# Performance work log

Hardware: AMD Instinct MI355X
Metric: run time of the kernel (lower is better)

## Reference

```python
import jax, jax.numpy as jnp
import numpy as np

B, S, IN_DIM = 8, 1024, 512
EMBED_DIM, NUM_HEADS = 512, 8
HEAD_DIM = EMBED_DIM // NUM_HEADS
LN_EPS = 1e-5


def setup_inputs() -> dict:
    key = jax.random.key(0)
    k1, k2, k3 = jax.random.split(key, 3)
    x = jax.random.normal(k1, (B, S, IN_DIM), dtype=jnp.float32)
    # xavier_uniform for qkv_proj.weight [3*embed, in] and o_proj.weight [embed, embed]
    lim_qkv = float(np.sqrt(6.0 / (3 * EMBED_DIM + IN_DIM)))
    w_qkv = jax.random.uniform(k2, (3 * EMBED_DIM, IN_DIM), dtype=jnp.float32,
                               minval=-lim_qkv, maxval=lim_qkv)
    lim_o = float(np.sqrt(6.0 / (EMBED_DIM + EMBED_DIM)))
    w_o = jax.random.uniform(k3, (EMBED_DIM, EMBED_DIM), dtype=jnp.float32,
                             minval=-lim_o, maxval=lim_o)
    return {"x": x, "w_qkv": w_qkv, "w_o": w_o}


def reference(x, w_qkv, w_o):
    b, s, _ = x.shape
    # fused QKV projection: [b, s, 3*embed]
    qkv = jnp.einsum('bsi,ei->bse', x, w_qkv)
    # [b, h, s, 3*head_dim]
    qkv = qkv.reshape(b, s, NUM_HEADS, 3 * HEAD_DIM).transpose(0, 2, 1, 3)
    q, k, v = jnp.split(qkv, 3, axis=-1)
    scale = 1.0 / np.sqrt(HEAD_DIM)
    logits = jnp.einsum('bhqd,bhkd->bhqk', q, k) * scale  # [b, h, s, s]
    attn = jax.nn.softmax(logits, axis=-1)
    vals = jnp.einsum('bhqk,bhkd->bhqd', attn, v)
    vals = vals.transpose(0, 2, 1, 3).reshape(b, s, EMBED_DIM)
    o = jnp.einsum('bse,fe->bsf', vals, w_o)
    # LayerNorm over [seq, embed] jointly (fresh nn.LayerNorm([N, D]): weight=1, bias=0)
    mu = jnp.mean(o, axis=(-2, -1), keepdims=True)
    var = jnp.var(o, axis=(-2, -1), keepdims=True)
    o = (o - mu) / jnp.sqrt(var + LN_EPS)
    return o
```

## Files before the change

kernel.cpp:

```cpp
#include <hip/hip_runtime.h>
#include <hip/hip_bf16.h>
#include <math.h>

#define BB 8
#define SS 1024
#define INDIM 512
#define ED 512
#define NH 8
#define HD 64

typedef __attribute__((ext_vector_type(8))) short short8;
typedef __attribute__((ext_vector_type(4))) float f32x4;
typedef __attribute__((ext_vector_type(16))) float f32x16;
typedef unsigned short u16;

typedef __attribute__((address_space(1))) const void gv_t;
typedef __attribute__((address_space(3))) void lv_t;

static __device__ __forceinline__ u16 f2bf(float f) {
  union { float f; unsigned u; } v; v.f = f;
  unsigned r = v.u + 0x7fffu + ((v.u >> 16) & 1u);
  return (u16)(r >> 16);
}

static __device__ __forceinline__ unsigned cvt_pk_bf16(float a, float b) {
  unsigned r;
  asm("v_cvt_pk_bf16_f32 %0, %1, %2" : "=v"(r) : "v"(a), "v"(b));
  return r;
}
static __device__ __forceinline__ float fast_exp2(float x) {
  float r; asm("v_exp_f32 %0, %1" : "=v"(r) : "v"(x)); return r;
}

__global__ void cvt_all(const float* __restrict__ x, const float* __restrict__ wq,
                        const float* __restrict__ wo, u16* __restrict__ xb,
                        u16* __restrict__ wqb, u16* __restrict__ wob) {
  const int n1 = 1048576;
  const int n2 = n1 + 196608;
  const int n3 = n2 + 65536;
  int i = blockIdx.x * blockDim.x + threadIdx.x;
  int stride = gridDim.x * blockDim.x;
  for (; i < n3; i += stride) {
    const float4* src; ushort4* dst; int j;
    if (i < n1)      { src = (const float4*)x;  dst = (ushort4*)xb;  j = i; }
    else if (i < n2) { src = (const float4*)wq; dst = (ushort4*)wqb; j = i - n1; }
    else             { src = (const float4*)wo; dst = (ushort4*)wob; j = i - n2; }
    float4 v = src[j];
    ushort4 o;
    o.x = f2bf(v.x); o.y = f2bf(v.y); o.z = f2bf(v.z); o.w = f2bf(v.w);
    dst[j] = o;
  }
}

template<int EPI>
__global__ __launch_bounds__(256, 2)
void gemm_nt(const u16* __restrict__ A, const u16* __restrict__ Bm, int K,
             float* __restrict__ outF,
             u16* __restrict__ qws, u16* __restrict__ kws, u16* __restrict__ vtws,
             float2* __restrict__ partials)
{
  __shared__ u16 As[128][64];
  __shared__ u16 Bs[128][64];
  const int tid = threadIdx.x;
  const int lane = tid & 63;
  const int wv = tid >> 6;
  const int wr = wv >> 1, wc = wv & 1;
  const int bm = blockIdx.x, bn = blockIdx.y;
  const int l15 = lane & 15, lg = lane >> 4;
  const int srow8 = lane >> 3;
  const int sc8 = lane & 7;

  f32x4 acc[4][4];
  #pragma unroll
  for (int i = 0; i < 4; i++)
    #pragma unroll
    for (int j = 0; j < 4; j++) acc[i][j] = (f32x4){0.f, 0.f, 0.f, 0.f};

  for (int kk = 0; kk < K; kk += 64) {
    #pragma unroll
    for (int i = 0; i < 4; i++) {
      int r0 = (i * 4 + wv) * 8;
      int r = r0 + srow8;
      int cs = sc8 ^ (r & 7);
      const u16* ga = A + (size_t)(bm * 128 + r) * K + kk + cs * 8;
      __builtin_amdgcn_global_load_lds((gv_t*)ga, (lv_t*)&As[r0][0], 16, 0, 0);
      const u16* gb = Bm + (size_t)(bn * 128 + r) * K + kk + cs * 8;
      __builtin_amdgcn_global_load_lds((gv_t*)gb, (lv_t*)&Bs[r0][0], 16, 0, 0);
    }
    __syncthreads();
    #pragma unroll
    for (int kc = 0; kc < 2; kc++) {
      short8 af[4], bf[4];
      #pragma unroll
      for (int mi = 0; mi < 4; mi++) {
        int ra = wr * 64 + mi * 16 + l15;
        af[mi] = *(const short8*)&As[ra][((kc * 4 + lg) ^ (ra & 7)) * 8];
      }
      #pragma unroll
      for (int ni = 0; ni < 4; ni++) {
        int rb = wc * 64 + ni * 16 + l15;
        bf[ni] = *(const short8*)&Bs[rb][((kc * 4 + lg) ^ (rb & 7)) * 8];
      }
      #pragma unroll
      for (int mi = 0; mi < 4; mi++)
        #pragma unroll
        for (int ni = 0; ni < 4; ni++)
          acc[mi][ni] = __builtin_amdgcn_mfma_f32_16x16x32_bf16(af[mi], bf[ni], acc[mi][ni], 0, 0, 0);
    }
    __syncthreads();
  }

  if (EPI == 0) {
    #pragma unroll
    for (int mi = 0; mi < 4; mi++) {
      int rowg = bm * 128 + wr * 64 + mi * 16 + lg * 4;
      #pragma unroll
      for (int ni = 0; ni < 4; ni++) {
        int colg = bn * 128 + wc * 64 + ni * 16 + l15;
        #pragma unroll
        for (int r = 0; r < 4; r++) {
          int rg = rowg + r;
          float v = acc[mi][ni][r];
          int b = rg >> 10, s = rg & 1023;
          int h = colg / 192, c = colg - h * 192;
          int bh = b * 8 + h;
          if (c < 64)
            qws[((size_t)(bh * 1024 + s)) * 64 + c] = f2bf(v * 0.18033688f);
          else if (c < 128)
            kws[((size_t)(bh * 1024 + s)) * 64 + (c - 64)] = f2bf(v);
          else
            vtws[((size_t)(bh * 64 + (c - 128))) * 1024 + s] = f2bf(v);
        }
      }
    }
  } else {
    float s1 = 0.f, s2 = 0.f;
    #pragma unroll
    for (int mi = 0; mi < 4; mi++) {
      int rowg = bm * 128 + wr * 64 + mi * 16 + lg * 4;
      #pragma unroll
      for (int ni = 0; ni < 4; ni++) {
        int colg = bn * 128 + wc * 64 + ni * 16 + l15;
        #pragma unroll
        for (int r = 0; r < 4; r++) {
          float v = acc[mi][ni][r];
          s1 += v; s2 += v * v;
          outF[(size_t)(rowg + r) * 512 + colg] = v;
        }
      }
    }
    #pragma unroll
    for (int off = 1; off < 64; off <<= 1) {
      s1 += __shfl_xor(s1, off);
      s2 += __shfl_xor(s2, off);
    }
    __shared__ float r1[4], r2[4];
    if (lane == 0) { r1[wv] = s1; r2[wv] = s2; }
    __syncthreads();
    if (tid == 0) {
      float t1 = r1[0] + r1[1] + r1[2] + r1[3];
      float t2 = r2[0] + r2[1] + r2[2] + r2[3];
      partials[bm * 4 + bn] = make_float2(t1, t2);
    }
  }
}

__global__ __launch_bounds__(512, 4)
void attn_kernel(const u16* __restrict__ qws, const u16* __restrict__ kws,
                 const u16* __restrict__ vtws, u16* __restrict__ vals)
{
  __shared__ __align__(16) u16 Ksm[2][64][72];
  __shared__ __align__(16) u16 Vsm[2][64][72];
  const int tid = threadIdx.x;
  const int lane = tid & 63;
  const int wq = tid >> 6;
  const int l31 = lane & 31;
  const int hi = lane >> 5;
  const int logical = (blockIdx.x & 7) * 32 + (blockIdx.x >> 3);
  const int bh = logical >> 2;
  const int q0 = (logical & 3) * 256;

  short8 qf[4];
  {
    const u16* qp = qws + ((size_t)bh * 1024 + q0 + wq * 32 + l31) * 64 + 8 * hi;
    #pragma unroll
    for (int j = 0; j < 4; j++) qf[j] = *(const short8*)(qp + 16 * j);
  }

  const int srow = tid >> 3;
  const int sc8 = (tid & 7) * 8;
  uint4 kreg, vreg;
  kreg = *(const uint4*)(kws + ((size_t)bh * 1024 + srow) * 64 + sc8);
  vreg = *(const uint4*)(vtws + ((size_t)(bh * 64 + srow)) * 1024 + sc8);
  *(uint4*)&Ksm[0][srow][sc8] = kreg;
  *(uint4*)&Vsm[0][srow][sc8] = vreg;
  __syncthreads();

  f32x16 o[2];
  #pragma unroll
  for (int r = 0; r < 16; r++) { o[0][r] = 0.f; o[1][r] = 0.f; }
  float m = -1e30f, l = 0.f;

  for (int t = 0; t < 16; t++) {
    const int cur = t & 1;
    if (t < 15) {
      int kv = (t + 1) * 64;
      kreg = *(const uint4*)(kws + ((size_t)bh * 1024 + kv + srow) * 64 + sc8);
      vreg = *(const uint4*)(vtws + ((size_t)(bh * 64 + srow)) * 1024 + kv + sc8);
    }

    f32x16 stv[2];
    __builtin_amdgcn_s_setprio(1);
    #pragma unroll
    for (int s2 = 0; s2 < 2; s2++) {
      f32x16 c;
      #pragma unroll
      for (int r = 0; r < 16; r++) c[r] = 0.f;
      #pragma unroll
      for (int j = 0; j < 4; j++) {
        short8 kf = *(const short8*)&Ksm[cur][s2 * 32 + l31][16 * j + 8 * hi];
        c = __builtin_amdgcn_mfma_f32_32x32x16_bf16(kf, qf[j], c, 0, 0, 0);
      }
      stv[s2] = c;
    }
    __builtin_amdgcn_s_setprio(0);

    float mx[16];
    #pragma unroll
    for (int r = 0; r < 16; r++) mx[r] = fmaxf(stv[0][r], stv[1][r]);
    #pragma unroll
    for (int w = 8; w >= 1; w >>= 1)
      #pragma unroll
      for (int r = 0; r < w; r++) mx[r] = fmaxf(mx[r], mx[r + w]);
    float pm = fmaxf(mx[0], __shfl_xor(mx[0], 32));

    if (!__all(pm - m <= 10.0f)) {
      float mn = fmaxf(m, pm);
      float al = fast_exp2(m - mn);
      m = mn; l *= al;
      #pragma unroll
      for (int reg = 0; reg < 16; reg++) {
        int qrow = (reg & 3) + 8 * (reg >> 2) + 4 * hi;
        float alo = __shfl(al, qrow);
        o[0][reg] *= alo; o[1][reg] *= alo;
      }
    }

    unsigned pk[16];
    float ps[16];
    #pragma unroll
    for (int s2 = 0; s2 < 2; s2++)
      #pragma unroll
      for (int j = 0; j < 8; j++) {
        float p0 = fast_exp2(stv[s2][2 * j] - m);
        float p1 = fast_exp2(stv[s2][2 * j + 1] - m);
        ps[s2 * 8 + j] = p0 + p1;
        pk[s2 * 8 + j] = cvt_pk_bf16(p0, p1);
      }
    #pragma unroll
    for (int w = 8; w >= 1; w >>= 1)
      #pragma unroll
      for (int r = 0; r < w; r++) ps[r] += ps[r + w];
    l += ps[0] + __shfl_xor(ps[0], 32);

    short8 pa[4];
    #pragma unroll
    for (int cc = 0; cc < 4; cc++) {
      int base = (cc >> 1) * 8 + (cc & 1) * 4;
      unsigned a0 = pk[base + 0], a2 = pk[base + 2];
      unsigned a1 = pk[base + 1], a3 = pk[base + 3];
      asm volatile("v_permlane32_swap_b32 %0, %1" : "+v"(a0), "+v"(a2));
      asm volatile("v_permlane32_swap_b32 %0, %1" : "+v"(a1), "+v"(a3));
      union { unsigned u[4]; short8 s8; } uu;
      uu.u[0] = a0; uu.u[1] = a1; uu.u[2] = a2; uu.u[3] = a3;
      pa[cc] = uu.s8;
    }

    __builtin_amdgcn_s_setprio(1);
    #pragma unroll
    for (int dh = 0; dh < 2; dh++)
      #pragma unroll
      for (int cc = 0; cc < 4; cc++) {
        short8 vf = *(const short8*)&Vsm[cur][dh * 32 + l31][16 * cc + 8 * hi];
        o[dh] = __builtin_amdgcn_mfma_f32_32x32x16_bf16(pa[cc], vf, o[dh], 0, 0, 0);
      }
    __builtin_amdgcn_s_setprio(0);

    if (t < 15) {
      *(uint4*)&Ksm[cur ^ 1][srow][sc8] = kreg;
      *(uint4*)&Vsm[cur ^ 1][srow][sc8] = vreg;
    }
    __syncthreads();
  }

  const int b = bh >> 3, h = bh & 7;
  #pragma unroll
  for (int reg = 0; reg < 16; reg++) {
    int qrow = (reg & 3) + 8 * (reg >> 2) + 4 * hi;
    float linv = 1.0f / __shfl(l, qrow);
    size_t grow = (size_t)(b * 1024 + q0 + wq * 32 + qrow) * 512 + h * 64;
    vals[grow + l31]      = f2bf(o[0][reg] * linv);
    vals[grow + 32 + l31] = f2bf(o[1][reg] * linv);
  }
}

__global__ void ln_norm2(float* __restrict__ o, const float2* __restrict__ partials) {
  const int blk = blockIdx.x;
  const int b = blk >> 8;
  const int lane = threadIdx.x & 63;
  float s1 = 0.f, s2 = 0.f;
  if (lane < 32) {
    float2 p = partials[b * 32 + lane];
    s1 = p.x; s2 = p.y;
  }
  #pragma unroll
  for (int off = 1; off < 64; off <<= 1) {
    s1 += __shfl_xor(s1, off);
    s2 += __shfl_xor(s2, off);
  }
  float mu = s1 / 524288.f;
  float rs = rsqrtf(s2 / 524288.f - mu * mu + 1e-5f);
  const int base = blk * 512;
  #pragma unroll
  for (int k = 0; k < 2; k++) {
    int i = base + threadIdx.x + k * 256;
    float4 v = ((const float4*)o)[i];
    v.x = (v.x - mu) * rs; v.y = (v.y - mu) * rs;
    v.z = (v.z - mu) * rs; v.w = (v.w - mu) * rs;
    ((float4*)o)[i] = v;
  }
}

extern "C" void kernel_launch(void* const* d_in, const int* in_sizes, int n_in,
                              void* d_out, int out_size, void* d_ws, size_t ws_size,
                              hipStream_t stream) {
  const float* x = (const float*)d_in[0];
  const float* wqkv = (const float*)d_in[1];
  const float* wo = (const float*)d_in[2];
  float* out = (float*)d_out;
  char* ws = (char*)d_ws;

  u16* xb        = (u16*)(ws + 0);
  u16* wqb       = (u16*)(ws + 8388608);
  u16* wob       = (u16*)(ws + 9961472);
  u16* qws       = (u16*)(ws + 10485760);
  u16* kws       = (u16*)(ws + 18874368);
  u16* vtws      = (u16*)(ws + 27262976);
  u16* vals      = (u16*)(ws + 35651584);
  float2* parts  = (float2*)(ws + 44040192);

  cvt_all<<<1280, 256, 0, stream>>>(x, wqkv, wo, xb, wqb, wob);

  dim3 g1(64, 12);
  gemm_nt<0><<<g1, 256, 0, stream>>>(xb, wqb, 512, nullptr, qws, kws, vtws, nullptr);

  attn_kernel<<<256, 512, 0, stream>>>(qws, kws, vtws, vals);

  dim3 g2(64, 4);
  gemm_nt<1><<<g2, 256, 0, stream>>>(vals, wob, 512, out, nullptr, nullptr, nullptr, parts);

  ln_norm2<<<2048, 256, 0, stream>>>(out, parts);
}
```

Before: 82.75 us.

## Double attention KV tile to 128 keys and interleave softmax with PV MFMAs

The attention kernel now processes 128 keys per iteration instead of 64, which halves the number of loop iterations and __syncthreads barriers and enlarges the double-buffered K/V shared-memory tiles. The exp/pack/PV work is split into per-32-key chunks so that probability conversion and PV MFMAs interleave, which keeps register pressure bounded. In exchange the kernel uses more LDS and registers, and launch bounds drop from 4 to 2 blocks per CU, so occupancy is lower.

Result: slower. 88.88 us (+7.4%).

```diff
diff --git a/kernel.cpp b/kernel.cpp
--- a/kernel.cpp
+++ b/kernel.cpp
@@ -165,12 +165,12 @@
   }
 }
 
-__global__ __launch_bounds__(512, 4)
+__global__ __launch_bounds__(512, 2)
 void attn_kernel(const u16* __restrict__ qws, const u16* __restrict__ kws,
                  const u16* __restrict__ vtws, u16* __restrict__ vals)
 {
-  __shared__ __align__(16) u16 Ksm[2][64][72];
-  __shared__ __align__(16) u16 Vsm[2][64][72];
+  __shared__ __align__(16) u16 Ksm[2][128][72];
+  __shared__ __align__(16) u16 Vsm[2][64][136];
   const int tid = threadIdx.x;
   const int lane = tid & 63;
   const int wq = tid >> 6;
@@ -189,11 +189,17 @@
 
   const int srow = tid >> 3;
   const int sc8 = (tid & 7) * 8;
-  uint4 kreg, vreg;
-  kreg = *(const uint4*)(kws + ((size_t)bh * 1024 + srow) * 64 + sc8);
-  vreg = *(const uint4*)(vtws + ((size_t)(bh * 64 + srow)) * 1024 + sc8);
-  *(uint4*)&Ksm[0][srow][sc8] = kreg;
-  *(uint4*)&Vsm[0][srow][sc8] = vreg;
+  const int vrow = tid >> 4;
+  const int vc8 = (tid & 15) * 8;
+  uint4 kreg[2], vreg[2];
+  kreg[0] = *(const uint4*)(kws + ((size_t)bh * 1024 + srow) * 64 + sc8);
+  kreg[1] = *(const uint4*)(kws + ((size_t)bh * 1024 + srow + 64) * 64 + sc8);
+  vreg[0] = *(const uint4*)(vtws + ((size_t)(bh * 64 + vrow)) * 1024 + vc8);
+  vreg[1] = *(const uint4*)(vtws + ((size_t)(bh * 64 + vrow + 32)) * 1024 + vc8);
+  *(uint4*)&Ksm[0][srow][sc8] = kreg[0];
+  *(uint4*)&Ksm[0][srow + 64][sc8] = kreg[1];
+  *(uint4*)&Vsm[0][vrow][vc8] = vreg[0];
+  *(uint4*)&Vsm[0][vrow + 32][vc8] = vreg[1];
   __syncthreads();
 
   f32x16 o[2];
@@ -201,18 +207,20 @@
   for (int r = 0; r < 16; r++) { o[0][r] = 0.f; o[1][r] = 0.f; }
   float m = -1e30f, l = 0.f;
 
-  for (int t = 0; t < 16; t++) {
+  for (int t = 0; t < 8; t++) {
     const int cur = t & 1;
-    if (t < 15) {
-      int kv = (t + 1) * 64;
-      kreg = *(const uint4*)(kws + ((size_t)bh * 1024 + kv + srow) * 64 + sc8);
-      vreg = *(const uint4*)(vtws + ((size_t)(bh * 64 + srow)) * 1024 + kv + sc8);
-    }
-
-    f32x16 stv[2];
+    if (t < 7) {
+      int kv = (t + 1) * 128;
+      kreg[0] = *(const uint4*)(kws + ((size_t)bh * 1024 + kv + srow) * 64 + sc8);
+      kreg[1] = *(const uint4*)(kws + ((size_t)bh * 1024 + kv + srow + 64) * 64 + sc8);
+      vreg[0] = *(const uint4*)(vtws + ((size_t)(bh * 64 + vrow)) * 1024 + kv + vc8);
+      vreg[1] = *(const uint4*)(vtws + ((size_t)(bh * 64 + vrow + 32)) * 1024 + kv + vc8);
+    }
+
+    f32x16 stv[4];
     __builtin_amdgcn_s_setprio(1);
     #pragma unroll
-    for (int s2 = 0; s2 < 2; s2++) {
+    for (int s2 = 0; s2 < 4; s2++) {
       f32x16 c;
       #pragma unroll
       for (int r = 0; r < 16; r++) c[r] = 0.f;
@@ -227,7 +235,8 @@
 
     float mx[16];
     #pragma unroll
-    for (int r = 0; r < 16; r++) mx[r] = fmaxf(stv[0][r], stv[1][r]);
+    for (int r = 0; r < 16; r++)
+      mx[r] = fmaxf(fmaxf(stv[0][r], stv[1][r]), fmaxf(stv[2][r], stv[3][r]));
     #pragma unroll
     for (int w = 8; w >= 1; w >>= 1)
       #pragma unroll
@@ -246,49 +255,53 @@
       }
     }
 
-    unsigned pk[16];
-    float ps[16];
-    #pragma unroll
-    for (int s2 = 0; s2 < 2; s2++)
+    float psum = 0.f;
+    #pragma unroll
+    for (int s2 = 0; s2 < 4; s2++) {
+      unsigned pkl[8];
+      float ps[8];
       #pragma unroll
       for (int j = 0; j < 8; j++) {
         float p0 = fast_exp2(stv[s2][2 * j] - m);
         float p1 = fast_exp2(stv[s2][2 * j + 1] - m);
-        ps[s2 * 8 + j] = p0 + p1;
-        pk[s2 * 8 + j] = cvt_pk_bf16(p0, p1);
-      }
-    #pragma unroll
-    for (int w = 8; w >= 1; w >>= 1)
-      #pragma unroll
-      for (int r = 0; r < w; r++) ps[r] += ps[r + w];
-    l += ps[0] + __shfl_xor(ps[0], 32);
-
-    short8 pa[4];
-    #pragma unroll
-    for (int cc = 0; cc < 4; cc++) {
-      int base = (cc >> 1) * 8 + (cc & 1) * 4;
-      unsigned a0 = pk[base + 0], a2 = pk[base + 2];
-      unsigned a1 = pk[base + 1], a3 = pk[base + 3];
-      asm volatile("v_permlane32_swap_b32 %0, %1" : "+v"(a0), "+v"(a2));
-      asm volatile("v_permlane32_swap_b32 %0, %1" : "+v"(a1), "+v"(a3));
-      union { unsigned u[4]; short8 s8; } uu;
-      uu.u[0] = a0; uu.u[1] = a1; uu.u[2] = a2; uu.u[3] = a3;
-      pa[cc] = uu.s8;
-    }
-
-    __builtin_amdgcn_s_setprio(1);
-    #pragma unroll
-    for (int dh = 0; dh < 2; dh++)
-      #pragma unroll
-      for (int cc = 0; cc < 4; cc++) {
-        short8 vf = *(const short8*)&Vsm[cur][dh * 32 + l31][16 * cc + 8 * hi];
-        o[dh] = __builtin_amdgcn_mfma_f32_32x32x16_bf16(pa[cc], vf, o[dh], 0, 0, 0);
-      }
-    __builtin_amdgcn_s_setprio(0);
-
-    if (t < 15) {
-      *(uint4*)&Ksm[cur ^ 1][srow][sc8] = kreg;
-      *(uint4*)&Vsm[cur ^ 1][srow][sc8] = vreg;
+        ps[j] = p0 + p1;
+        pkl[j] = cvt_pk_bf16(p0, p1);
+      }
+      #pragma unroll
+      for (int w = 4; w >= 1; w >>= 1)
+        #pragma unroll
+        for (int r = 0; r < w; r++) ps[r] += ps[r + w];
+      psum += ps[0];
+
+      short8 pa[2];
+      #pragma unroll
+      for (int cc = 0; cc < 2; cc++) {
+        unsigned a0 = pkl[cc * 4 + 0], a2 = pkl[cc * 4 + 2];
+        unsigned a1 = pkl[cc * 4 + 1], a3 = pkl[cc * 4 + 3];
+        asm volatile("v_permlane32_swap_b32 %0, %1" : "+v"(a0), "+v"(a2));
+        asm volatile("v_permlane32_swap_b32 %0, %1" : "+v"(a1), "+v"(a3));
+        union { unsigned u[4]; short8 s8; } uu;
+        uu.u[0] = a0; uu.u[1] = a1; uu.u[2] = a2; uu.u[3] = a3;
+        pa[cc] = uu.s8;
+      }
+
+      __builtin_amdgcn_s_setprio(1);
+      #pragma unroll
+      for (int dh = 0; dh < 2; dh++)
+        #pragma unroll
+        for (int cc = 0; cc < 2; cc++) {
+          short8 vf = *(const short8*)&Vsm[cur][dh * 32 + l31][16 * (s2 * 2 + cc) + 8 * hi];
+          o[dh] = __builtin_amdgcn_mfma_f32_32x32x16_bf16(pa[cc], vf, o[dh], 0, 0, 0);
+        }
+      __builtin_amdgcn_s_setprio(0);
+    }
+    l += psum + __shfl_xor(psum, 32);
+
+    if (t < 7) {
+      *(uint4*)&Ksm[cur ^ 1][srow][sc8] = kreg[0];
+      *(uint4*)&Ksm[cur ^ 1][srow + 64][sc8] = kreg[1];
+      *(uint4*)&Vsm[cur ^ 1][vrow][vc8] = vreg[0];
+      *(uint4*)&Vsm[cur ^ 1][vrow + 32][vc8] = vreg[1];
     }
     __syncthreads();
   }
```

## Split attention KV range in two and merge partial outputs with a combine kernel

Applied to the files above, without the earlier changes.

Attention blocks now use 256 threads, 128 query rows, and half of the key/value sequence each, giving 1024 blocks instead of 256. Each block writes a normalized bf16 partial output and its running max and sum. A new merge kernel rescales and combines the two halves into the final values layout. This raises parallelism so more CUs stay busy, but adds a kernel launch, extra global traffic for the partials, and an extra bf16 rounding step.

Result: slower. 92.08 us (+11.3%).

```diff
diff --git a/kernel.cpp b/kernel.cpp
--- a/kernel.cpp
+++ b/kernel.cpp
@@ -165,9 +165,10 @@
   }
 }
 
-__global__ __launch_bounds__(512, 4)
+__global__ __launch_bounds__(256, 4)
 void attn_kernel(const u16* __restrict__ qws, const u16* __restrict__ kws,
-                 const u16* __restrict__ vtws, u16* __restrict__ vals)
+                 const u16* __restrict__ vtws, u16* __restrict__ opart,
+                 float2* __restrict__ mlbuf)
 {
   __shared__ __align__(16) u16 Ksm[2][64][72];
   __shared__ __align__(16) u16 Vsm[2][64][72];
@@ -176,9 +177,12 @@
   const int wq = tid >> 6;
   const int l31 = lane & 31;
   const int hi = lane >> 5;
-  const int logical = (blockIdx.x & 7) * 32 + (blockIdx.x >> 3);
-  const int bh = logical >> 2;
-  const int q0 = (logical & 3) * 256;
+  const int logical = (blockIdx.x & 7) * 128 + (blockIdx.x >> 3);
+  const int bh = logical >> 4;
+  const int qt = (logical >> 1) & 7;
+  const int half = logical & 1;
+  const int q0 = qt * 128;
+  const int kv0 = half * 512;
 
   short8 qf[4];
   {
@@ -189,11 +193,15 @@
 
   const int srow = tid >> 3;
   const int sc8 = (tid & 7) * 8;
-  uint4 kreg, vreg;
-  kreg = *(const uint4*)(kws + ((size_t)bh * 1024 + srow) * 64 + sc8);
-  vreg = *(const uint4*)(vtws + ((size_t)(bh * 64 + srow)) * 1024 + sc8);
-  *(uint4*)&Ksm[0][srow][sc8] = kreg;
-  *(uint4*)&Vsm[0][srow][sc8] = vreg;
+  uint4 kreg[2], vreg[2];
+  kreg[0] = *(const uint4*)(kws + ((size_t)bh * 1024 + kv0 + srow) * 64 + sc8);
+  kreg[1] = *(const uint4*)(kws + ((size_t)bh * 1024 + kv0 + srow + 32) * 64 + sc8);
+  vreg[0] = *(const uint4*)(vtws + ((size_t)(bh * 64 + srow)) * 1024 + kv0 + sc8);
+  vreg[1] = *(const uint4*)(vtws + ((size_t)(bh * 64 + srow + 32)) * 1024 + kv0 + sc8);
+  *(uint4*)&Ksm[0][srow][sc8] = kreg[0];
+  *(uint4*)&Ksm[0][srow + 32][sc8] = kreg[1];
+  *(uint4*)&Vsm[0][srow][sc8] = vreg[0];
+  *(uint4*)&Vsm[0][srow + 32][sc8] = vreg[1];
   __syncthreads();
 
   f32x16 o[2];
@@ -201,12 +209,14 @@
   for (int r = 0; r < 16; r++) { o[0][r] = 0.f; o[1][r] = 0.f; }
   float m = -1e30f, l = 0.f;
 
-  for (int t = 0; t < 16; t++) {
+  for (int t = 0; t < 8; t++) {
     const int cur = t & 1;
-    if (t < 15) {
-      int kv = (t + 1) * 64;
-      kreg = *(const uint4*)(kws + ((size_t)bh * 1024 + kv + srow) * 64 + sc8);
-      vreg = *(const uint4*)(vtws + ((size_t)(bh * 64 + srow)) * 1024 + kv + sc8);
+    if (t < 7) {
+      int kv = kv0 + (t + 1) * 64;
+      kreg[0] = *(const uint4*)(kws + ((size_t)bh * 1024 + kv + srow) * 64 + sc8);
+      kreg[1] = *(const uint4*)(kws + ((size_t)bh * 1024 + kv + srow + 32) * 64 + sc8);
+      vreg[0] = *(const uint4*)(vtws + ((size_t)(bh * 64 + srow)) * 1024 + kv + sc8);
+      vreg[1] = *(const uint4*)(vtws + ((size_t)(bh * 64 + srow + 32)) * 1024 + kv + sc8);
     }
 
     f32x16 stv[2];
@@ -286,22 +296,68 @@
       }
     __builtin_amdgcn_s_setprio(0);
 
-    if (t < 15) {
-      *(uint4*)&Ksm[cur ^ 1][srow][sc8] = kreg;
-      *(uint4*)&Vsm[cur ^ 1][srow][sc8] = vreg;
+    if (t < 7) {
+      *(uint4*)&Ksm[cur ^ 1][srow][sc8] = kreg[0];
+      *(uint4*)&Ksm[cur ^ 1][srow + 32][sc8] = kreg[1];
+      *(uint4*)&Vsm[cur ^ 1][srow][sc8] = vreg[0];
+      *(uint4*)&Vsm[cur ^ 1][srow + 32][sc8] = vreg[1];
     }
     __syncthreads();
   }
 
-  const int b = bh >> 3, h = bh & 7;
+  const size_t qbase = (size_t)half * 65536 + (size_t)bh * 1024 + q0 + wq * 32;
+  if (hi == 0)
+    mlbuf[qbase + l31] = make_float2(m, l);
   #pragma unroll
   for (int reg = 0; reg < 16; reg++) {
     int qrow = (reg & 3) + 8 * (reg >> 2) + 4 * hi;
     float linv = 1.0f / __shfl(l, qrow);
-    size_t grow = (size_t)(b * 1024 + q0 + wq * 32 + qrow) * 512 + h * 64;
-    vals[grow + l31]      = f2bf(o[0][reg] * linv);
-    vals[grow + 32 + l31] = f2bf(o[1][reg] * linv);
-  }
+    size_t grow = (qbase + qrow) * 64;
+    opart[grow + l31]      = f2bf(o[0][reg] * linv);
+    opart[grow + 32 + l31] = f2bf(o[1][reg] * linv);
+  }
+}
+
+__global__ void attn_merge(const u16* __restrict__ opart,
+                           const float2* __restrict__ mlbuf,
+                           u16* __restrict__ vals)
+{
+  int idx = blockIdx.x * 256 + threadIdx.x;
+  int q = idx >> 3;
+  int d8 = (idx & 7) * 8;
+  float2 ml0 = mlbuf[q];
+  float2 ml1 = mlbuf[65536 + q];
+  float M = fmaxf(ml0.x, ml1.x);
+  float w0 = ml0.y * fast_exp2(ml0.x - M);
+  float w1 = ml1.y * fast_exp2(ml1.x - M);
+  float inv = 1.0f / (w0 + w1);
+  w0 *= inv; w1 *= inv;
+  ushort4 a0 = *(const ushort4*)(opart + (size_t)q * 64 + d8);
+  ushort4 a1 = *(const ushort4*)(opart + (size_t)q * 64 + d8 + 4);
+  ushort4 b0 = *(const ushort4*)(opart + (size_t)(65536 + q) * 64 + d8);
+  ushort4 b1 = *(const ushort4*)(opart + (size_t)(65536 + q) * 64 + d8 + 4);
+  const u16* ap = (const u16*)&a0;
+  ushort4 o0, o1;
+  {
+    u16 av[8] = {a0.x, a0.y, a0.z, a0.w, a1.x, a1.y, a1.z, a1.w};
+    u16 bv[8] = {b0.x, b0.y, b0.z, b0.w, b1.x, b1.y, b1.z, b1.w};
+    u16 ov[8];
+    #pragma unroll
+    for (int j = 0; j < 8; j++) {
+      union { unsigned u; float f; } fa, fb;
+      fa.u = (unsigned)av[j] << 16;
+      fb.u = (unsigned)bv[j] << 16;
+      ov[j] = f2bf(w0 * fa.f + w1 * fb.f);
+    }
+    o0 = make_ushort4(ov[0], ov[1], ov[2], ov[3]);
+    o1 = make_ushort4(ov[4], ov[5], ov[6], ov[7]);
+  }
+  (void)ap;
+  int bh = q >> 10, s = q & 1023;
+  int b = bh >> 3, h = bh & 7;
+  size_t vbase = ((size_t)(b * 1024 + s)) * 512 + h * 64 + d8;
+  *(ushort4*)(vals + vbase) = o0;
+  *(ushort4*)(vals + vbase + 4) = o1;
 }
 
 __global__ void ln_norm2(float* __restrict__ o, const float2* __restrict__ partials) {
@@ -346,15 +402,18 @@
   u16* qws       = (u16*)(ws + 10485760);
   u16* kws       = (u16*)(ws + 18874368);
   u16* vtws      = (u16*)(ws + 27262976);
-  u16* vals      = (u16*)(ws + 35651584);
-  float2* parts  = (float2*)(ws + 44040192);
+  u16* opart     = (u16*)(ws + 35651584);
+  float2* mlbuf  = (float2*)(ws + 52428800);
+  u16* vals      = (u16*)(ws + 53477376);
+  float2* parts  = (float2*)(ws + 61865984);
 
   cvt_all<<<1280, 256, 0, stream>>>(x, wqkv, wo, xb, wqb, wob);
 
   dim3 g1(64, 12);
   gemm_nt<0><<<g1, 256, 0, stream>>>(xb, wqb, 512, nullptr, qws, kws, vtws, nullptr);
 
-  attn_kernel<<<256, 512, 0, stream>>>(qws, kws, vtws, vals);
+  attn_kernel<<<1024, 256, 0, stream>>>(qws, kws, vtws, opart, mlbuf);
+  attn_merge<<<2048, 256, 0, stream>>>(opart, mlbuf, vals);
 
   dim3 g2(64, 4);
   gemm_nt<1><<<g2, 256, 0, stream>>>(vals, wob, 512, out, nullptr, nullptr, nullptr, parts);
```
